# Kernel tuning notes

Measured on AMD Instinct MI355X. Metric: run time of the kernel, lower is better.

## Reference

```python
import jax, jax.numpy as jnp
import numpy as np

H = 256          # hidden size per direction (lstm_hdn_size // 2)
EPS = 1e-5       # BatchNorm1d eps


def _lstm_cell_step(x, w_ih, w_hh, b_ih, b_hh):
    # Single-timestep LSTM cell with zero initial (h, c). seq_len == 1 so both
    # directions reduce to one cell step. x: [N, in], w_ih: [4H, in], w_hh: [4H, H]
    h0 = jnp.zeros((x.shape[0], H), x.dtype)
    gates = x @ w_ih.T + b_ih + h0 @ w_hh.T + b_hh   # [N, 4H], torch gate order i,f,g,o
    i, f, g, o = jnp.split(gates, 4, axis=-1)
    c = jax.nn.sigmoid(i) * jnp.tanh(g)              # f * c0 == 0
    h = jax.nn.sigmoid(o) * jnp.tanh(c)
    return h


def _emission(x, bn_gamma, bn_beta, w_ih_l0, w_hh_l0, b_ih_l0, b_hh_l0,
              w_ih_l1, w_hh_l1, b_ih_l1, b_hh_l1, fc_w, fc_b):
    # x: [N, 1, D]; BatchNorm1d over channel D, training-mode batch statistics
    mu = jnp.mean(x, axis=(0, 1))
    var = jnp.var(x, axis=(0, 1))
    b = (x - mu) * jax.lax.rsqrt(var + EPS) * bn_gamma + bn_beta
    b = b[:, 0, :]                                   # squeeze seq_len == 1 -> [N, D]
    # bidirectional layer 0 (both directions see the same single timestep)
    h0f = _lstm_cell_step(b, w_ih_l0[0], w_hh_l0[0], b_ih_l0[0], b_hh_l0[0])
    h0b = _lstm_cell_step(b, w_ih_l0[1], w_hh_l0[1], b_ih_l0[1], b_hh_l0[1])
    h1_in = jnp.concatenate([h0f, h0b], axis=-1)     # [N, 2H]
    # bidirectional layer 1 (inter-layer LSTM dropout = identity in eval)
    h1f = _lstm_cell_step(h1_in, w_ih_l1[0], w_hh_l1[0], b_ih_l1[0], b_hh_l1[0])
    h1b = _lstm_cell_step(h1_in, w_ih_l1[1], w_hh_l1[1], b_ih_l1[1], b_hh_l1[1])
    h = jnp.concatenate([h1f, h1b], axis=-1)         # [N, 2H]
    # Dropout(p) is identity in eval; fc1 -> 2 tags
    return h @ fc_w.T + fc_b                          # [N, 2]


def _crf_nll(e, tags, crf_start, crf_end, crf_trans):
    # torchcrf CRF negative log-likelihood, chain length N, batch 1, full mask.
    # e: [N, 2], tags: [N]
    N = e.shape[0]
    num = (crf_start[tags[0]] + jnp.sum(e[jnp.arange(N), tags])
           + jnp.sum(crf_trans[tags[:-1], tags[1:]]) + crf_end[tags[-1]])
    def step(alpha, et):
        alpha = jax.nn.logsumexp(alpha[:, None] + crf_trans, axis=0) + et
        return alpha, None
    alpha0 = crf_start + e[0]
    alphaN, _ = jax.lax.scan(step, alpha0, e[1:])
    den = jax.nn.logsumexp(alphaN + crf_end)
    return -(num - den)                               # loss = -crf(emissions, tags)


def setup_inputs():
    key = jax.random.key(0)
    ks = jax.random.split(key, 16)
    N, D = 65536, 768
    s = 0.05
    return {
        "x": jax.random.normal(ks[0], (N, 1, D), jnp.float32),
        "bn_gamma": jnp.ones((D,), jnp.float32),
        "bn_beta": jnp.zeros((D,), jnp.float32),
        "w_ih_l0": jax.random.normal(ks[1], (2, 4 * H, D), jnp.float32) * s,
        "w_hh_l0": jax.random.normal(ks[2], (2, 4 * H, H), jnp.float32) * s,
        "b_ih_l0": jax.random.normal(ks[3], (2, 4 * H), jnp.float32) * s,
        "b_hh_l0": jax.random.normal(ks[4], (2, 4 * H), jnp.float32) * s,
        "w_ih_l1": jax.random.normal(ks[5], (2, 4 * H, 2 * H), jnp.float32) * s,
        "w_hh_l1": jax.random.normal(ks[6], (2, 4 * H, H), jnp.float32) * s,
        "b_ih_l1": jax.random.normal(ks[7], (2, 4 * H), jnp.float32) * s,
        "b_hh_l1": jax.random.normal(ks[8], (2, 4 * H), jnp.float32) * s,
        "fc_w": jax.random.normal(ks[9], (2, 2 * H), jnp.float32) * s,
        "fc_b": jnp.zeros((2,), jnp.float32),
        "crf_start": jax.random.normal(ks[10], (2,), jnp.float32) * s,
        "crf_end": jax.random.normal(ks[11], (2,), jnp.float32) * s,
        "crf_trans": jax.random.normal(ks[12], (2, 2), jnp.float32) * s,
        "labels": jax.random.randint(ks[13], (N,), 0, 2),
    }


def reference(x, bn_gamma, bn_beta, w_ih_l0, w_hh_l0, b_ih_l0, b_hh_l0,
              w_ih_l1, w_hh_l1, b_ih_l1, b_hh_l1, fc_w, fc_b,
              crf_start, crf_end, crf_trans, labels):
    e = _emission(x, bn_gamma, bn_beta, w_ih_l0, w_hh_l0, b_ih_l0, b_hh_l0,
                  w_ih_l1, w_hh_l1, b_ih_l1, b_hh_l1, fc_w, fc_b)
    loss = _crf_nll(e, labels, crf_start, crf_end, crf_trans)
    logits = e[:, None, :]   # [N, 1, 2], matches torch `emission`
    return loss, logits
```

## Files before the change

kernel.cpp:

```cpp
#include <hip/hip_runtime.h>

typedef _Float16 f16x8 __attribute__((ext_vector_type(8)));
typedef _Float16 f16x4 __attribute__((ext_vector_type(4)));
typedef float f32x4 __attribute__((ext_vector_type(4)));

static constexpr int NROWS = 65536;

static constexpr size_t OB_BG0  = 0;
static constexpr size_t OB_BG1  = OB_BG0 + 6144;
static constexpr size_t OB_W1H  = OB_BG1 + 6144;
static constexpr size_t OB_W1L  = OB_W1H + 2359296;
static constexpr size_t OB_W2H  = OB_W1L + 2359296;
static constexpr size_t OB_W2L  = OB_W2H + 1572864;
static constexpr size_t OB_E    = OB_W2L + 1572864;
static constexpr size_t OB_PMAT = OB_E + 524288;
static constexpr size_t OB_NUM  = OB_PMAT + 16384;
static constexpr size_t OB_HH   = OB_NUM + 256;
static constexpr size_t OB_HL   = OB_HH + 67108864;
static constexpr size_t OB_PSUM  = OB_HH;
static constexpr size_t OB_PSUM2 = OB_PSUM + 786432;
static constexpr size_t OB_SF    = OB_PSUM2 + 786432;
static constexpr size_t OB_TF    = OB_SF + 3072;

__device__ __forceinline__ float sigm_(float x) { return 1.f / (1.f + __expf(-x)); }
__device__ __forceinline__ float tanh_(float x) {
  x = fminf(fmaxf(x, -15.f), 15.f);
  float e = __expf(2.f * x);
  return (e - 1.f) / (e + 1.f);
}
__device__ __forceinline__ float lse2_(float a, float b) {
  float m = fmaxf(a, b);
  float d = fabsf(a - b);
  return m + log1pf(expf(-d));
}
__device__ __forceinline__ void gload16(const void* g, void* l) {
  __builtin_amdgcn_global_load_lds(
      (const __attribute__((address_space(1))) void*)g,
      (__attribute__((address_space(3))) void*)l, 16, 0, 0);
}

__global__ __launch_bounds__(256) void bn_partial(const float* __restrict__ x,
                                                  float* __restrict__ psum,
                                                  float* __restrict__ psum2) {
  int d = blockIdx.x * 256 + threadIdx.x;
  int chunk = blockIdx.y;
  const float* p = x + (size_t)chunk * 256 * 768 + d;
  float s = 0.f, s2 = 0.f;
  #pragma unroll 8
  for (int r = 0; r < 256; ++r) {
    float v = p[(size_t)r * 768];
    s += v;
    s2 = fmaf(v, v, s2);
  }
  psum[(size_t)chunk * 768 + d] = s;
  psum2[(size_t)chunk * 768 + d] = s2;
}

__global__ __launch_bounds__(256) void bn_finalize(const float* __restrict__ gamma,
                                                   const float* __restrict__ beta,
                                                   const float* __restrict__ psum,
                                                   const float* __restrict__ psum2,
                                                   float* __restrict__ sf_out,
                                                   float* __restrict__ tf_out) {
  int d = blockIdx.x * 256 + threadIdx.x;
  float s = 0.f, s2 = 0.f;
  for (int c = 0; c < 256; ++c) {
    s  += psum[(size_t)c * 768 + d];
    s2 += psum2[(size_t)c * 768 + d];
  }
  float mu  = s  * (1.f / NROWS);
  float var = s2 * (1.f / NROWS) - mu * mu;
  float sf  = rsqrtf(var + 1e-5f) * gamma[d];
  sf_out[d] = sf;
  tf_out[d] = beta[d] - mu * sf;
}

__global__ __launch_bounds__(256) void prep_w0(const float* __restrict__ w,
                                               const float* __restrict__ b_ih,
                                               const float* __restrict__ b_hh,
                                               const float* __restrict__ sf,
                                               const float* __restrict__ tf,
                                               _Float16* __restrict__ wh,
                                               _Float16* __restrict__ wl,
                                               float* __restrict__ bg) {
  int q = blockIdx.x;
  int s = q >> 9, j = q & 511, dir = j >> 8, jj = j & 255;
  int goff = (s == 0) ? 0 : ((s == 1) ? 512 : 768);
  int row = dir * 1024 + goff + jj;
  const float* src = w + (size_t)row * 768;
  float acc = 0.f;
  for (int d = threadIdx.x; d < 768; d += 256) {
    float wv = src[d];
    float wf = wv * sf[d];
    _Float16 h = (_Float16)wf;
    wh[(size_t)q * 768 + d] = h;
    wl[(size_t)q * 768 + d] = (_Float16)(wf - (float)h);
    acc = fmaf(wv, tf[d], acc);
  }
  for (int off = 32; off; off >>= 1) acc += __shfl_down(acc, off);
  __shared__ float red[4];
  if ((threadIdx.x & 63) == 0) red[threadIdx.x >> 6] = acc;
  __syncthreads();
  if (threadIdx.x == 0)
    bg[q] = red[0] + red[1] + red[2] + red[3] + b_ih[row] + b_hh[row];
}

__global__ __launch_bounds__(256) void prep_w1(const float* __restrict__ w,
                                               const float* __restrict__ b_ih,
                                               const float* __restrict__ b_hh,
                                               _Float16* __restrict__ wh,
                                               _Float16* __restrict__ wl,
                                               float* __restrict__ bg) {
  int q = blockIdx.x;
  int s = q >> 9, j = q & 511, dir = j >> 8, jj = j & 255;
  int goff = (s == 0) ? 0 : ((s == 1) ? 512 : 768);
  int row = dir * 1024 + goff + jj;
  const float* src = w + (size_t)row * 512;
  for (int d = threadIdx.x; d < 512; d += 256) {
    float wv = src[d];
    _Float16 h = (_Float16)wv;
    wh[(size_t)q * 512 + d] = h;
    wl[(size_t)q * 512 + d] = (_Float16)(wv - (float)h);
  }
  if (threadIdx.x == 0) bg[q] = b_ih[row] + b_hh[row];
}

__global__ __launch_bounds__(256) void init_misc(const float* __restrict__ fc_b,
                                                 float* __restrict__ e,
                                                 float* __restrict__ num) {
  int i = blockIdx.x * 256 + threadIdx.x;
  if (i < NROWS * 2) e[i] = fc_b[i & 1];
  if (i == 0) num[0] = 0.f;
}

__device__ __forceinline__ void mfma_core(const _Float16 (*Ah)[32], const _Float16 (*Al)[32],
                                          const _Float16 (*Bh)[32], const _Float16 (*Bl)[32],
                                          int wm, int wc, int l15, int lhi,
                                          f32x4 acc[4][3][2]) {
  f16x8 ah[4], al[4];
  #pragma unroll
  for (int mf = 0; mf < 4; ++mf) {
    ah[mf] = *(const f16x8*)&Ah[wm * 64 + mf * 16 + l15][lhi * 8];
    al[mf] = *(const f16x8*)&Al[wm * 64 + mf * 16 + l15][lhi * 8];
  }
  #pragma unroll
  for (int s = 0; s < 3; ++s)
    #pragma unroll
    for (int jf = 0; jf < 2; ++jf) {
      int br = s * 64 + wc * 32 + jf * 16 + l15;
      f16x8 bh = *(const f16x8*)&Bh[br][lhi * 8];
      f16x8 bl = *(const f16x8*)&Bl[br][lhi * 8];
      #pragma unroll
      for (int mf = 0; mf < 4; ++mf) {
        acc[mf][s][jf] = __builtin_amdgcn_mfma_f32_16x16x32_f16(ah[mf], bh, acc[mf][s][jf], 0, 0, 0);
        acc[mf][s][jf] = __builtin_amdgcn_mfma_f32_16x16x32_f16(ah[mf], bl, acc[mf][s][jf], 0, 0, 0);
        acc[mf][s][jf] = __builtin_amdgcn_mfma_f32_16x16x32_f16(al[mf], bh, acc[mf][s][jf], 0, 0, 0);
      }
    }
}

__global__ __launch_bounds__(256, 2) void gemm1(const float* __restrict__ A,
                                                const _Float16* __restrict__ Wh,
                                                const _Float16* __restrict__ Wl,
                                                const float* __restrict__ bg,
                                                _Float16* __restrict__ Hh,
                                                _Float16* __restrict__ Hl) {
  constexpr int K = 768;
  __shared__ __align__(16) _Float16 Ah[128][32], Al[128][32];
  __shared__ __align__(16) _Float16 Bh[192][32], Bl[192][32];

  const int tid = threadIdx.x;
  const int lane = tid & 63, wvid = tid >> 6;
  const int l15 = lane & 15, lhi = lane >> 4;
  const int wm = wvid >> 1, wc = wvid & 1;

  int bid = blockIdx.y * 8 + blockIdx.x;
  int wid = (bid & 7) * 512 + (bid >> 3);
  const int m0 = (wid >> 3) * 128;
  const int c0 = (wid & 7) * 64;

  f32x4 acc[4][3][2] = {};

  for (int k0 = 0; k0 < K; k0 += 32) {
    #pragma unroll
    for (int p = 0; p < 4; ++p) {
      int i = tid + p * 256;
      int row = i >> 3, cc4 = i & 7;
      const float4 v = *(const float4*)(A + (size_t)(m0 + row) * K + k0 + cc4 * 4);
      f16x4 hv, lv;
      hv[0] = (_Float16)v.x; lv[0] = (_Float16)(v.x - (float)hv[0]);
      hv[1] = (_Float16)v.y; lv[1] = (_Float16)(v.y - (float)hv[1]);
      hv[2] = (_Float16)v.z; lv[2] = (_Float16)(v.z - (float)hv[2]);
      hv[3] = (_Float16)v.w; lv[3] = (_Float16)(v.w - (float)hv[3]);
      *(f16x4*)&Ah[row][cc4 * 4] = hv;
      *(f16x4*)&Al[row][cc4 * 4] = lv;
    }
    #pragma unroll
    for (int it = 0; it < 3; ++it) {
      int g = wvid + it * 4;
      int idx = g * 64 + lane;
      int brow = idx >> 2, kp = idx & 3;
      int s = brow >> 6, j = brow & 63;
      size_t off = (size_t)(s * 512 + c0 + j) * K + (k0 + kp * 8);
      gload16(Wh + off, (char*)Bh + g * 1024);
      gload16(Wl + off, (char*)Bl + g * 1024);
    }
    __syncthreads();
    mfma_core(Ah, Al, Bh, Bl, wm, wc, l15, lhi, acc);
    __syncthreads();
  }

  const int rb = m0 + wm * 64 + lhi * 4;
  #pragma unroll
  for (int mf = 0; mf < 4; ++mf)
    #pragma unroll
    for (int jf = 0; jf < 2; ++jf) {
      const int hcol = c0 + wc * 32 + jf * 16 + l15;
      const float bi = bg[hcol], bgv = bg[512 + hcol], bo = bg[1024 + hcol];
      #pragma unroll
      for (int r = 0; r < 4; ++r) {
        float gi = acc[mf][0][jf][r] + bi;
        float gg = acc[mf][1][jf][r] + bgv;
        float go = acc[mf][2][jf][r] + bo;
        float cv = sigm_(gi) * tanh_(gg);
        float h  = sigm_(go) * tanh_(cv);
        size_t o = (size_t)(rb + mf * 16 + r) * 512 + hcol;
        _Float16 hh = (_Float16)h;
        Hh[o] = hh;
        Hl[o] = (_Float16)(h - (float)hh);
      }
    }
}

__global__ __launch_bounds__(256, 2) void gemm2(const _Float16* __restrict__ Ahg,
                                                const _Float16* __restrict__ Alg,
                                                const _Float16* __restrict__ Wh,
                                                const _Float16* __restrict__ Wl,
                                                const float* __restrict__ bg,
                                                const float* __restrict__ fcw,
                                                float* __restrict__ ew) {
  constexpr int K = 512;
  __shared__ __align__(16) _Float16 Ah[128][32], Al[128][32];
  __shared__ __align__(16) _Float16 Bh[192][32], Bl[192][32];

  const int tid = threadIdx.x;
  const int lane = tid & 63, wvid = tid >> 6;
  const int l15 = lane & 15, lhi = lane >> 4;
  const int wm = wvid >> 1, wc = wvid & 1;

  int bid = blockIdx.y * 8 + blockIdx.x;
  int wid = (bid & 7) * 512 + (bid >> 3);
  const int m0 = (wid >> 3) * 128;
  const int c0 = (wid & 7) * 64;

  f32x4 acc[4][3][2] = {};

  for (int k0 = 0; k0 < K; k0 += 32) {
    #pragma unroll
    for (int it = 0; it < 2; ++it) {
      int g = wvid + it * 4;
      int idx = g * 64 + lane;
      int row = idx >> 2, kp = idx & 3;
      size_t off = (size_t)(m0 + row) * K + (k0 + kp * 8);
      gload16(Ahg + off, (char*)Ah + g * 1024);
      gload16(Alg + off, (char*)Al + g * 1024);
    }
    #pragma unroll
    for (int it = 0; it < 3; ++it) {
      int g = wvid + it * 4;
      int idx = g * 64 + lane;
      int brow = idx >> 2, kp = idx & 3;
      int s = brow >> 6, j = brow & 63;
      size_t off = (size_t)(s * 512 + c0 + j) * K + (k0 + kp * 8);
      gload16(Wh + off, (char*)Bh + g * 1024);
      gload16(Wl + off, (char*)Bl + g * 1024);
    }
    __syncthreads();
    mfma_core(Ah, Al, Bh, Bl, wm, wc, l15, lhi, acc);
    __syncthreads();
  }

  const int rb = m0 + wm * 64 + lhi * 4;
  #pragma unroll
  for (int mf = 0; mf < 4; ++mf) {
    float pe0[4] = {0.f, 0.f, 0.f, 0.f}, pe1[4] = {0.f, 0.f, 0.f, 0.f};
    #pragma unroll
    for (int jf = 0; jf < 2; ++jf) {
      const int hcol = c0 + wc * 32 + jf * 16 + l15;
      const float bi = bg[hcol], bgv = bg[512 + hcol], bo = bg[1024 + hcol];
      const float f0 = fcw[hcol], f1 = fcw[512 + hcol];
      #pragma unroll
      for (int r = 0; r < 4; ++r) {
        float gi = acc[mf][0][jf][r] + bi;
        float gg = acc[mf][1][jf][r] + bgv;
        float go = acc[mf][2][jf][r] + bo;
        float cv = sigm_(gi) * tanh_(gg);
        float h  = sigm_(go) * tanh_(cv);
        pe0[r] = fmaf(h, f0, pe0[r]);
        pe1[r] = fmaf(h, f1, pe1[r]);
      }
    }
    #pragma unroll
    for (int r = 0; r < 4; ++r) {
      float a0 = pe0[r], a1 = pe1[r];
      #pragma unroll
      for (int off = 1; off < 16; off <<= 1) {
        a0 += __shfl_xor(a0, off);
        a1 += __shfl_xor(a1, off);
      }
      if (l15 == 0) {
        int rowg = rb + mf * 16 + r;
        atomicAdd(&ew[(size_t)rowg * 2 + 0], a0);
        atomicAdd(&ew[(size_t)rowg * 2 + 1], a1);
      }
    }
  }
}

__global__ __launch_bounds__(256) void crf_partial(const float* __restrict__ ew,
                                                   const int* __restrict__ labels,
                                                   const float* __restrict__ trans,
                                                   float* __restrict__ pmat,
                                                   float* __restrict__ numacc) {
  int g = blockIdx.x * 256 + threadIdx.x;
  int t0 = 1 + g * 64;
  int t1 = t0 + 64; if (t1 > NROWS) t1 = NROWS;
  const float t00 = trans[0], t01 = trans[1], t10 = trans[2], t11 = trans[3];
  float p00 = 0.f, p01 = -1e30f, p10 = -1e30f, p11 = 0.f;
  float num = 0.f;
  int prev = labels[t0 - 1];
  for (int t = t0; t < t1; ++t) {
    float e0 = ew[(size_t)t * 2], e1 = ew[(size_t)t * 2 + 1];
    float m00 = t00 + e0, m01 = t01 + e1, m10 = t10 + e0, m11 = t11 + e1;
    float n00 = lse2_(p00 + m00, p01 + m10);
    float n01 = lse2_(p00 + m01, p01 + m11);
    float n10 = lse2_(p10 + m00, p11 + m10);
    float n11 = lse2_(p10 + m01, p11 + m11);
    p00 = n00; p01 = n01; p10 = n10; p11 = n11;
    int cur = labels[t];
    num += (cur ? e1 : e0) + trans[prev * 2 + cur];
    prev = cur;
  }
  float* pm = pmat + (size_t)g * 4;
  pm[0] = p00; pm[1] = p01; pm[2] = p10; pm[3] = p11;
  for (int off = 32; off; off >>= 1) num += __shfl_down(num, off);
  if ((threadIdx.x & 63) == 0) atomicAdd(numacc, num);
}

__global__ __launch_bounds__(256) void crf_final(const float* __restrict__ ew,
                                                 const int* __restrict__ labels,
                                                 const float* __restrict__ cstart,
                                                 const float* __restrict__ cend,
                                                 const float* __restrict__ pmat,
                                                 const float* __restrict__ numacc,
                                                 float* __restrict__ out) {
  __shared__ float sm[256][4];
  int t = threadIdx.x;
  const float* pm = pmat + (size_t)t * 16;
  float p00 = pm[0], p01 = pm[1], p10 = pm[2], p11 = pm[3];
  #pragma unroll
  for (int u = 1; u < 4; ++u) {
    const float* q = pm + u * 4;
    float b00 = q[0], b01 = q[1], b10 = q[2], b11 = q[3];
    float n00 = lse2_(p00 + b00, p01 + b10);
    float n01 = lse2_(p00 + b01, p01 + b11);
    float n10 = lse2_(p10 + b00, p11 + b10);
    float n11 = lse2_(p10 + b01, p11 + b11);
    p00 = n00; p01 = n01; p10 = n10; p11 = n11;
  }
  sm[t][0] = p00; sm[t][1] = p01; sm[t][2] = p10; sm[t][3] = p11;
  __syncthreads();
  for (int s = 1; s < 256; s <<= 1) {
    int i = t * (s << 1);
    if (i + s < 256) {
      float a00 = sm[i][0], a01 = sm[i][1], a10 = sm[i][2], a11 = sm[i][3];
      float b00 = sm[i + s][0], b01 = sm[i + s][1], b10 = sm[i + s][2], b11 = sm[i + s][3];
      sm[i][0] = lse2_(a00 + b00, a01 + b10);
      sm[i][1] = lse2_(a00 + b01, a01 + b11);
      sm[i][2] = lse2_(a10 + b00, a11 + b10);
      sm[i][3] = lse2_(a10 + b01, a11 + b11);
    }
    __syncthreads();
  }
  if (t == 0) {
    float a0 = cstart[0] + ew[0];
    float a1 = cstart[1] + ew[1];
    float aN0 = lse2_(a0 + sm[0][0], a1 + sm[0][2]);
    float aN1 = lse2_(a0 + sm[0][1], a1 + sm[0][3]);
    float den = lse2_(aN0 + cend[0], aN1 + cend[1]);
    int tag0 = labels[0], tagN = labels[NROWS - 1];
    float num = numacc[0] + cstart[tag0] + ew[tag0] + cend[tagN];
    out[0] = den - num;
  }
}

__global__ __launch_bounds__(256) void copy_logits(const float* __restrict__ ew,
                                                   float* __restrict__ out) {
  int i = blockIdx.x * 256 + threadIdx.x;
  if (i < NROWS * 2) out[1 + i] = ew[i];
}

extern "C" void kernel_launch(void* const* d_in, const int* in_sizes, int n_in,
                              void* d_out, int out_size, void* d_ws, size_t ws_size,
                              hipStream_t stream) {
  const float* x        = (const float*)d_in[0];
  const float* gamma    = (const float*)d_in[1];
  const float* beta     = (const float*)d_in[2];
  const float* w_ih_l0  = (const float*)d_in[3];
  const float* b_ih_l0  = (const float*)d_in[5];
  const float* b_hh_l0  = (const float*)d_in[6];
  const float* w_ih_l1  = (const float*)d_in[7];
  const float* b_ih_l1  = (const float*)d_in[9];
  const float* b_hh_l1  = (const float*)d_in[10];
  const float* fc_w     = (const float*)d_in[11];
  const float* fc_b     = (const float*)d_in[12];
  const float* crf_start= (const float*)d_in[13];
  const float* crf_end  = (const float*)d_in[14];
  const float* crf_trans= (const float*)d_in[15];
  const int*   labels   = (const int*)d_in[16];

  char* ws   = (char*)d_ws;
  float* out = (float*)d_out;

  float*     bg0  = (float*)(ws + OB_BG0);
  float*     bg1  = (float*)(ws + OB_BG1);
  _Float16*  w1h  = (_Float16*)(ws + OB_W1H);
  _Float16*  w1l  = (_Float16*)(ws + OB_W1L);
  _Float16*  w2h  = (_Float16*)(ws + OB_W2H);
  _Float16*  w2l  = (_Float16*)(ws + OB_W2L);
  float*     e    = (float*)(ws + OB_E);
  float*     pmat = (float*)(ws + OB_PMAT);
  float*     num  = (float*)(ws + OB_NUM);
  _Float16*  hh   = (_Float16*)(ws + OB_HH);
  _Float16*  hl   = (_Float16*)(ws + OB_HL);
  float*     psum = (float*)(ws + OB_PSUM);
  float*     psum2= (float*)(ws + OB_PSUM2);
  float*     sf   = (float*)(ws + OB_SF);
  float*     tf   = (float*)(ws + OB_TF);

  bn_partial<<<dim3(3, 256), 256, 0, stream>>>(x, psum, psum2);
  bn_finalize<<<3, 256, 0, stream>>>(gamma, beta, psum, psum2, sf, tf);
  prep_w0<<<1536, 256, 0, stream>>>(w_ih_l0, b_ih_l0, b_hh_l0, sf, tf, w1h, w1l, bg0);
  prep_w1<<<1536, 256, 0, stream>>>(w_ih_l1, b_ih_l1, b_hh_l1, w2h, w2l, bg1);
  init_misc<<<512, 256, 0, stream>>>(fc_b, e, num);

  gemm1<<<dim3(8, 512), 256, 0, stream>>>(x, w1h, w1l, bg0, hh, hl);
  gemm2<<<dim3(8, 512), 256, 0, stream>>>(hh, hl, w2h, w2l, bg1, fc_w, e);

  crf_partial<<<4, 256, 0, stream>>>(e, labels, crf_trans, pmat, num);
  crf_final<<<1, 256, 0, stream>>>(e, labels, crf_start, crf_end, pmat, num, out);
  copy_logits<<<512, 256, 0, stream>>>(e, out);
}
```

Measured before the change: 1.266 ms.

## Pre-tile weights into MFMA fragment layout and widen K-step to 64

Weights are written in prep kernels in a fragment-major tiled layout, so each B-tile load is a contiguous 1KB chunk per wave that maps directly to the MFMA lane layout. The K loop now steps by 64 with two MFMA sub-steps per barrier pair, halving synchronisation. The intermediate hidden state is stored as fp32 and split into fp16 hi/lo inside gemm2's staging instead of being pre-split into two fp16 arrays. This also lifts the LDS footprint per block, which may limit occupancy.

Result: slower. 1.346 ms (+6.3%).

```diff
diff --git a/kernel.cpp b/kernel.cpp
--- a/kernel.cpp
+++ b/kernel.cpp
@@ -15,9 +15,8 @@
 static constexpr size_t OB_E    = OB_W2L + 1572864;
 static constexpr size_t OB_PMAT = OB_E + 524288;
 static constexpr size_t OB_NUM  = OB_PMAT + 16384;
-static constexpr size_t OB_HH   = OB_NUM + 256;
-static constexpr size_t OB_HL   = OB_HH + 67108864;
-static constexpr size_t OB_PSUM  = OB_HH;
+static constexpr size_t OB_H    = OB_NUM + 256;
+static constexpr size_t OB_PSUM  = OB_H;
 static constexpr size_t OB_PSUM2 = OB_PSUM + 786432;
 static constexpr size_t OB_SF    = OB_PSUM2 + 786432;
 static constexpr size_t OB_TF    = OB_SF + 3072;
@@ -37,6 +36,11 @@
   __builtin_amdgcn_global_load_lds(
       (const __attribute__((address_space(1))) void*)g,
       (__attribute__((address_space(3))) void*)l, 16, 0, 0);
+}
+
+__device__ __forceinline__ size_t wf_off(int q, int k, int K) {
+  return ((size_t)(q >> 4) * (K >> 5) + (k >> 5)) * 512 +
+         (size_t)(((k >> 3) & 3) * 128 + (q & 15) * 8 + (k & 7));
 }
 
 __global__ __launch_bounds__(256) void bn_partial(const float* __restrict__ x,
@@ -93,8 +97,9 @@
     float wv = src[d];
     float wf = wv * sf[d];
     _Float16 h = (_Float16)wf;
-    wh[(size_t)q * 768 + d] = h;
-    wl[(size_t)q * 768 + d] = (_Float16)(wf - (float)h);
+    size_t o = wf_off(q, d, 768);
+    wh[o] = h;
+    wl[o] = (_Float16)(wf - (float)h);
     acc = fmaf(wv, tf[d], acc);
   }
   for (int off = 32; off; off >>= 1) acc += __shfl_down(acc, off);
@@ -119,8 +124,9 @@
   for (int d = threadIdx.x; d < 512; d += 256) {
     float wv = src[d];
     _Float16 h = (_Float16)wv;
-    wh[(size_t)q * 512 + d] = h;
-    wl[(size_t)q * 512 + d] = (_Float16)(wv - (float)h);
+    size_t o = wf_off(q, d, 512);
+    wh[o] = h;
+    wl[o] = (_Float16)(wv - (float)h);
   }
   if (threadIdx.x == 0) bg[q] = b_ih[row] + b_hh[row];
 }
@@ -133,80 +139,108 @@
   if (i == 0) num[0] = 0.f;
 }
 
-__device__ __forceinline__ void mfma_core(const _Float16 (*Ah)[32], const _Float16 (*Al)[32],
-                                          const _Float16 (*Bh)[32], const _Float16 (*Bl)[32],
-                                          int wm, int wc, int l15, int lhi,
+__device__ __forceinline__ void mfma_step(const char* AhB, const char* AlB,
+                                          const char* BhB, const char* BlB,
+                                          int lane16, int wm, int wc,
                                           f32x4 acc[4][3][2]) {
-  f16x8 ah[4], al[4];
-  #pragma unroll
-  for (int mf = 0; mf < 4; ++mf) {
-    ah[mf] = *(const f16x8*)&Ah[wm * 64 + mf * 16 + l15][lhi * 8];
-    al[mf] = *(const f16x8*)&Al[wm * 64 + mf * 16 + l15][lhi * 8];
-  }
-  #pragma unroll
-  for (int s = 0; s < 3; ++s)
+  #pragma unroll
+  for (int kk = 0; kk < 2; ++kk) {
+    f16x8 ah[4], al[4];
     #pragma unroll
-    for (int jf = 0; jf < 2; ++jf) {
-      int br = s * 64 + wc * 32 + jf * 16 + l15;
-      f16x8 bh = *(const f16x8*)&Bh[br][lhi * 8];
-      f16x8 bl = *(const f16x8*)&Bl[br][lhi * 8];
+    for (int mf = 0; mf < 4; ++mf) {
+      int ln = ((wm * 4 + mf) * 2 + kk) * 1024 + lane16;
+      ah[mf] = *(const f16x8*)(AhB + ln);
+      al[mf] = *(const f16x8*)(AlB + ln);
+    }
+    #pragma unroll
+    for (int s = 0; s < 3; ++s)
       #pragma unroll
-      for (int mf = 0; mf < 4; ++mf) {
-        acc[mf][s][jf] = __builtin_amdgcn_mfma_f32_16x16x32_f16(ah[mf], bh, acc[mf][s][jf], 0, 0, 0);
-        acc[mf][s][jf] = __builtin_amdgcn_mfma_f32_16x16x32_f16(ah[mf], bl, acc[mf][s][jf], 0, 0, 0);
-        acc[mf][s][jf] = __builtin_amdgcn_mfma_f32_16x16x32_f16(al[mf], bh, acc[mf][s][jf], 0, 0, 0);
+      for (int jf = 0; jf < 2; ++jf) {
+        int ln = ((s * 4 + wc * 2 + jf) * 2 + kk) * 1024 + lane16;
+        f16x8 bh = *(const f16x8*)(BhB + ln);
+        f16x8 bl = *(const f16x8*)(BlB + ln);
+        #pragma unroll
+        for (int mf = 0; mf < 4; ++mf) {
+          acc[mf][s][jf] = __builtin_amdgcn_mfma_f32_16x16x32_f16(ah[mf], bh, acc[mf][s][jf], 0, 0, 0);
+          acc[mf][s][jf] = __builtin_amdgcn_mfma_f32_16x16x32_f16(ah[mf], bl, acc[mf][s][jf], 0, 0, 0);
+          acc[mf][s][jf] = __builtin_amdgcn_mfma_f32_16x16x32_f16(al[mf], bh, acc[mf][s][jf], 0, 0, 0);
+        }
       }
-    }
+  }
+}
+
+template <int K>
+__device__ __forceinline__ void stage_A(const float* __restrict__ Arow0,
+                                        int k0, int tid,
+                                        char* AhB, char* AlB) {
+  #pragma unroll
+  for (int p = 0; p < 4; ++p) {
+    int idx = p * 256 + tid;
+    int row = idx >> 3, ks = idx & 7;
+    const float* src = Arow0 + (size_t)row * K + k0 + ks * 8;
+    const float4 v0 = *(const float4*)src;
+    const float4 v1 = *(const float4*)(src + 4);
+    f16x8 hv, lv;
+    hv[0] = (_Float16)v0.x; lv[0] = (_Float16)(v0.x - (float)hv[0]);
+    hv[1] = (_Float16)v0.y; lv[1] = (_Float16)(v0.y - (float)hv[1]);
+    hv[2] = (_Float16)v0.z; lv[2] = (_Float16)(v0.z - (float)hv[2]);
+    hv[3] = (_Float16)v0.w; lv[3] = (_Float16)(v0.w - (float)hv[3]);
+    hv[4] = (_Float16)v1.x; lv[4] = (_Float16)(v1.x - (float)hv[4]);
+    hv[5] = (_Float16)v1.y; lv[5] = (_Float16)(v1.y - (float)hv[5]);
+    hv[6] = (_Float16)v1.z; lv[6] = (_Float16)(v1.z - (float)hv[6]);
+    hv[7] = (_Float16)v1.w; lv[7] = (_Float16)(v1.w - (float)hv[7]);
+    int waddr = ((row >> 4) * 2 + (ks >> 2)) * 1024 + (ks & 3) * 256 + (row & 15) * 16;
+    *(f16x8*)(AhB + waddr) = hv;
+    *(f16x8*)(AlB + waddr) = lv;
+  }
+}
+
+template <int K>
+__device__ __forceinline__ void stage_B(const _Float16* __restrict__ Wh,
+                                        const _Float16* __restrict__ Wl,
+                                        int c0, int k0, int wvid, int lane,
+                                        char* BhB, char* BlB) {
+  const int lane8 = lane * 8;
+  #pragma unroll
+  for (int it = 0; it < 6; ++it) {
+    int l24 = wvid + it * 4;
+    int kh = l24 & 1, srb = l24 >> 1;
+    int s = srb >> 2, rb = srb & 3;
+    int grb = s * 32 + (c0 >> 4) + rb;
+    size_t src = ((size_t)grb * (K >> 5) + (k0 >> 5) + kh) * 512 + lane8;
+    gload16(Wh + src, BhB + l24 * 1024);
+    gload16(Wl + src, BlB + l24 * 1024);
+  }
 }
 
 __global__ __launch_bounds__(256, 2) void gemm1(const float* __restrict__ A,
                                                 const _Float16* __restrict__ Wh,
                                                 const _Float16* __restrict__ Wl,
                                                 const float* __restrict__ bg,
-                                                _Float16* __restrict__ Hh,
-                                                _Float16* __restrict__ Hl) {
+                                                float* __restrict__ H) {
   constexpr int K = 768;
-  __shared__ __align__(16) _Float16 Ah[128][32], Al[128][32];
-  __shared__ __align__(16) _Float16 Bh[192][32], Bl[192][32];
+  __shared__ __align__(16) char AhB[16384], AlB[16384];
+  __shared__ __align__(16) char BhB[24576], BlB[24576];
 
   const int tid = threadIdx.x;
   const int lane = tid & 63, wvid = tid >> 6;
   const int l15 = lane & 15, lhi = lane >> 4;
   const int wm = wvid >> 1, wc = wvid & 1;
+  const int lane16 = lane * 16;
 
   int bid = blockIdx.y * 8 + blockIdx.x;
   int wid = (bid & 7) * 512 + (bid >> 3);
   const int m0 = (wid >> 3) * 128;
   const int c0 = (wid & 7) * 64;
+  const float* Arow0 = A + (size_t)m0 * K;
 
   f32x4 acc[4][3][2] = {};
 
-  for (int k0 = 0; k0 < K; k0 += 32) {
-    #pragma unroll
-    for (int p = 0; p < 4; ++p) {
-      int i = tid + p * 256;
-      int row = i >> 3, cc4 = i & 7;
-      const float4 v = *(const float4*)(A + (size_t)(m0 + row) * K + k0 + cc4 * 4);
-      f16x4 hv, lv;
-      hv[0] = (_Float16)v.x; lv[0] = (_Float16)(v.x - (float)hv[0]);
-      hv[1] = (_Float16)v.y; lv[1] = (_Float16)(v.y - (float)hv[1]);
-      hv[2] = (_Float16)v.z; lv[2] = (_Float16)(v.z - (float)hv[2]);
-      hv[3] = (_Float16)v.w; lv[3] = (_Float16)(v.w - (float)hv[3]);
-      *(f16x4*)&Ah[row][cc4 * 4] = hv;
-      *(f16x4*)&Al[row][cc4 * 4] = lv;
-    }
-    #pragma unroll
-    for (int it = 0; it < 3; ++it) {
-      int g = wvid + it * 4;
-      int idx = g * 64 + lane;
-      int brow = idx >> 2, kp = idx & 3;
-      int s = brow >> 6, j = brow & 63;
-      size_t off = (size_t)(s * 512 + c0 + j) * K + (k0 + kp * 8);
-      gload16(Wh + off, (char*)Bh + g * 1024);
-      gload16(Wl + off, (char*)Bl + g * 1024);
-    }
+  for (int k0 = 0; k0 < K; k0 += 64) {
+    stage_B<K>(Wh, Wl, c0, k0, wvid, lane, BhB, BlB);
+    stage_A<K>(Arow0, k0, tid, AhB, AlB);
     __syncthreads();
-    mfma_core(Ah, Al, Bh, Bl, wm, wc, l15, lhi, acc);
+    mfma_step(AhB, AlB, BhB, BlB, lane16, wm, wc, acc);
     __syncthreads();
   }
 
@@ -223,60 +257,40 @@
         float gg = acc[mf][1][jf][r] + bgv;
         float go = acc[mf][2][jf][r] + bo;
         float cv = sigm_(gi) * tanh_(gg);
-        float h  = sigm_(go) * tanh_(cv);
-        size_t o = (size_t)(rb + mf * 16 + r) * 512 + hcol;
-        _Float16 hh = (_Float16)h;
-        Hh[o] = hh;
-        Hl[o] = (_Float16)(h - (float)hh);
+        H[(size_t)(rb + mf * 16 + r) * 512 + hcol] = sigm_(go) * tanh_(cv);
       }
     }
 }
 
-__global__ __launch_bounds__(256, 2) void gemm2(const _Float16* __restrict__ Ahg,
-                                                const _Float16* __restrict__ Alg,
+__global__ __launch_bounds__(256, 2) void gemm2(const float* __restrict__ A,
                                                 const _Float16* __restrict__ Wh,
                                                 const _Float16* __restrict__ Wl,
                                                 const float* __restrict__ bg,
                                                 const float* __restrict__ fcw,
                                                 float* __restrict__ ew) {
   constexpr int K = 512;
-  __shared__ __align__(16) _Float16 Ah[128][32], Al[128][32];
-  __shared__ __align__(16) _Float16 Bh[192][32], Bl[192][32];
+  __shared__ __align__(16) char AhB[16384], AlB[16384];
+  __shared__ __align__(16) char BhB[24576], BlB[24576];
 
   const int tid = threadIdx.x;
   const int lane = tid & 63, wvid = tid >> 6;
   const int l15 = lane & 15, lhi = lane >> 4;
   const int wm = wvid >> 1, wc = wvid & 1;
+  const int lane16 = lane * 16;
 
   int bid = blockIdx.y * 8 + blockIdx.x;
   int wid = (bid & 7) * 512 + (bid >> 3);
   const int m0 = (wid >> 3) * 128;
   const int c0 = (wid & 7) * 64;
+  const float* Arow0 = A + (size_t)m0 * K;
 
   f32x4 acc[4][3][2] = {};
 
-  for (int k0 = 0; k0 < K; k0 += 32) {
-    #pragma unroll
-    for (int it = 0; it < 2; ++it) {
-      int g = wvid + it * 4;
-      int idx = g * 64 + lane;
-      int row = idx >> 2, kp = idx & 3;
-      size_t off = (size_t)(m0 + row) * K + (k0 + kp * 8);
-      gload16(Ahg + off, (char*)Ah + g * 1024);
-      gload16(Alg + off, (char*)Al + g * 1024);
-    }
-    #pragma unroll
-    for (int it = 0; it < 3; ++it) {
-      int g = wvid + it * 4;
-      int idx = g * 64 + lane;
-      int brow = idx >> 2, kp = idx & 3;
-      int s = brow >> 6, j = brow & 63;
-      size_t off = (size_t)(s * 512 + c0 + j) * K + (k0 + kp * 8);
-      gload16(Wh + off, (char*)Bh + g * 1024);
-      gload16(Wl + off, (char*)Bl + g * 1024);
-    }
+  for (int k0 = 0; k0 < K; k0 += 64) {
+    stage_B<K>(Wh, Wl, c0, k0, wvid, lane, BhB, BlB);
+    stage_A<K>(Arow0, k0, tid, AhB, AlB);
     __syncthreads();
-    mfma_core(Ah, Al, Bh, Bl, wm, wc, l15, lhi, acc);
+    mfma_step(AhB, AlB, BhB, BlB, lane16, wm, wc, acc);
     __syncthreads();
   }
 
@@ -431,8 +445,7 @@
   float*     e    = (float*)(ws + OB_E);
   float*     pmat = (float*)(ws + OB_PMAT);
   float*     num  = (float*)(ws + OB_NUM);
-  _Float16*  hh   = (_Float16*)(ws + OB_HH);
-  _Float16*  hl   = (_Float16*)(ws + OB_HL);
+  float*     H    = (float*)(ws + OB_H);
   float*     psum = (float*)(ws + OB_PSUM);
   float*     psum2= (float*)(ws + OB_PSUM2);
   float*     sf   = (float*)(ws + OB_SF);
@@ -444,8 +457,8 @@
   prep_w1<<<1536, 256, 0, stream>>>(w_ih_l1, b_ih_l1, b_hh_l1, w2h, w2l, bg1);
   init_misc<<<512, 256, 0, stream>>>(fc_b, e, num);
 
-  gemm1<<<dim3(8, 512), 256, 0, stream>>>(x, w1h, w1l, bg0, hh, hl);
-  gemm2<<<dim3(8, 512), 256, 0, stream>>>(hh, hl, w2h, w2l, bg1, fc_w, e);
+  gemm1<<<dim3(8, 512), 256, 0, stream>>>(x, w1h, w1l, bg0, H);
+  gemm2<<<dim3(8, 512), 256, 0, stream>>>(H, w2h, w2l, bg1, fc_w, e);
 
   crf_partial<<<4, 256, 0, stream>>>(e, labels, crf_trans, pmat, num);
   crf_final<<<1, 256, 0, stream>>>(e, labels, crf_start, crf_end, pmat, num, out);
```
